# Performance work log

Measured on AMD Instinct MI355X. Metric: run time of the kernel, lower is better.

## Reference

```python
import jax, jax.numpy as jnp
import numpy as np

N = 131072
L = 300  # lan_vec_len

def _boxes(k):
    k1, k2, k3, k4 = jax.random.split(k, 4)
    x1 = jax.random.uniform(k1, (N,)) * 500.0
    y1 = jax.random.uniform(k2, (N,)) * 500.0
    w = 1.0 + jax.random.uniform(k3, (N,)) * 200.0
    h = 1.0 + jax.random.uniform(k4, (N,)) * 200.0
    return x1, y1, x1 + w, y1 + h

def setup_inputs() -> dict:
    key = jax.random.key(0)
    ks = jax.random.split(key, 10)
    sbj_vec = jax.random.normal(ks[0], (N, L), jnp.float32)
    obj_vec = jax.random.normal(ks[1], (N, L), jnp.float32)
    sx1, sy1, sx2, sy2 = _boxes(ks[2])
    ox1, oy1, ox2, oy2 = _boxes(ks[3])
    label = jax.random.randint(ks[4], (N,), 0, 2).astype(jnp.float32)
    misc = jax.random.uniform(ks[5], (N,))
    # rlts columns: [0:4 misc, 4 label, 5:9 sbj box, 9 misc, 10:14 obj box, 14 misc]
    rlts = jnp.stack([misc, misc, misc, misc, label,
                      sx1, sy1, sx2, sy2, misc,
                      ox1, oy1, ox2, oy2, misc], axis=1)
    spa_w = jax.random.normal(ks[6], (8, 1), jnp.float32) * 0.1
    spa_b = jnp.zeros((1,), jnp.float32)
    lan_w1 = jax.random.normal(ks[7], (2 * L, L), jnp.float32) * 0.05
    lan_b1 = jnp.zeros((L,), jnp.float32)
    lan_w2 = jax.random.normal(ks[8], (L, 1), jnp.float32) * 0.05
    lan_b2 = jnp.zeros((1,), jnp.float32)
    return {"sbj_vec": sbj_vec, "obj_vec": obj_vec, "rlts": rlts,
            "spa_w": spa_w, "spa_b": spa_b,
            "lan_w1": lan_w1, "lan_b1": lan_b1,
            "lan_w2": lan_w2, "lan_b2": lan_b2}

def _ext_box_feat(rlts):
    sb = rlts[:, 5:9]
    ob = rlts[:, 10:14]
    sw = sb[:, 2] - sb[:, 0]
    sh = sb[:, 3] - sb[:, 1]
    ow = ob[:, 2] - ob[:, 0]
    oh = ob[:, 3] - ob[:, 1]
    sbj = jnp.stack([(sb[:, 0] - ob[:, 0]) / sw,
                     (sb[:, 1] - ob[:, 1]) / sh,
                     jnp.log(sw / ow), jnp.log(sh / oh)], axis=1)
    obj = jnp.stack([(ob[:, 0] - sb[:, 0]) / ow,
                     (ob[:, 1] - sb[:, 1]) / oh,
                     jnp.log(ow / sw), jnp.log(oh / sh)], axis=1)
    return sbj, obj

def reference(sbj_vec, obj_vec, rlts, spa_w, spa_b, lan_w1, lan_b1, lan_w2, lan_b2):
    sbj_box, obj_box = _ext_box_feat(rlts)
    lan_feat = jnp.concatenate([sbj_vec, obj_vec], axis=1)        # [N, 2L]
    box_feat = jnp.concatenate([sbj_box, obj_box], axis=1)        # [N, 8]
    # lan_stream: ReLU -> (Dropout: identity in eval) -> Linear -> ReLU -> Linear
    h = jax.nn.relu(lan_feat)
    h = jax.nn.relu(h @ lan_w1 + lan_b1)
    lan_scores = h @ lan_w2 + lan_b2                              # [N, 1]
    box_scores = box_feat @ spa_w + spa_b                         # [N, 1]
    scores = jax.nn.sigmoid(lan_scores + box_scores)              # [N, 1]
    ys = (rlts[:, 4] > 0).astype(scores.dtype)                    # [N]
    s = scores[:, 0]
    # binary cross entropy (mean), clamped like torch's BCE
    log_s = jnp.clip(jnp.log(jnp.clip(s, 1e-12, 1.0)), -100.0)
    log_1s = jnp.clip(jnp.log(jnp.clip(1.0 - s, 1e-12, 1.0)), -100.0)
    loss = -jnp.mean(ys * log_s + (1.0 - ys) * log_1s)
    # faithful replication of loss_test's (buggy) counting logic, vectorized
    neg = ys == 0
    pos = ~neg
    N_pos = jnp.sum(pos.astype(jnp.float32))
    N_neg = jnp.sum(neg.astype(jnp.float32))
    N_pos_right = jnp.sum((neg & (s >= 0.5)).astype(jnp.float32))
    N_neg_right = jnp.sum((pos & (s < 0.5)).astype(jnp.float32))
    recall_pos = N_pos_right / N_pos
    recall_neg = N_neg_right / N_neg
    recall_all = (N_pos_right + N_neg_right) / (N_pos + N_neg)
    return scores, loss, recall_pos, recall_neg, recall_all
```

## Files before the change

### kernel.cpp

```cpp
#include <hip/hip_runtime.h>

constexpr int NROWS  = 131072;
constexpr int LDIM   = 300;
constexpr int KDIM   = 600;
constexpr int NPAD   = 320;
constexpr int KGRP   = 76;
constexpr int MTILE  = 64;
constexpr int NBLKS  = NROWS / MTILE;
constexpr int KSTEPS = 19;
constexpr int WT_ELEMS = KGRP * NPAD * 8;
constexpr size_t PART_OFF = 393216;
constexpr int ASTRIDE = 40;

typedef __bf16 bf16x8 __attribute__((ext_vector_type(8)));
typedef float  f32x4  __attribute__((ext_vector_type(4)));

__device__ __forceinline__ unsigned short f2bf(float f) {
    unsigned u = __float_as_uint(f);
    u += 0x7fffu + ((u >> 16) & 1u);
    return (unsigned short)(u >> 16);
}

__global__ void prep_w1(const float* __restrict__ w1, unsigned short* __restrict__ wt) {
    int idx = blockIdx.x * 256 + threadIdx.x;
    if (idx >= WT_ELEMS) return;
    int j    = idx & 7;
    int rest = idx >> 3;
    int n    = rest % NPAD;
    int kg   = rest / NPAD;
    int k    = kg * 8 + j;
    float v = 0.f;
    if (k < KDIM && n < LDIM) v = w1[k * LDIM + n];
    wt[idx] = f2bf(v);
}

__launch_bounds__(256, 3)
__global__ void main_kernel(const float* __restrict__ sbj, const float* __restrict__ obj,
                            const float* __restrict__ rlts,
                            const float* __restrict__ spa_w, const float* __restrict__ spa_b,
                            const float* __restrict__ b1, const float* __restrict__ w2,
                            const float* __restrict__ b2,
                            const unsigned short* __restrict__ wt,
                            float* __restrict__ out_scores, float* __restrict__ part) {
    __shared__ __attribute__((aligned(16))) short A_lds[2][MTILE * ASTRIDE];
    __shared__ float lanpart[4][MTILE];
    __shared__ float redbuf[4][8];

    const int tid  = threadIdx.x;
    const int lane = tid & 63;
    const int wv   = tid >> 6;
    const int l4   = lane & 15;
    const int q4   = lane >> 4;
    const int nbase = wv * 80;

    const int  blk  = blockIdx.x;
    const long row0 = (long)blk * MTILE;

    const int a_quad = tid & 7;
    const int a_row  = tid >> 3;

    f32x4 acc[4][5];
    #pragma unroll
    for (int rt = 0; rt < 4; ++rt)
        #pragma unroll
        for (int ct = 0; ct < 5; ++ct)
            acc[rt][ct] = (f32x4)(0.f);

    float4 pre[2];

    auto load_A = [&](int kt) {
        const int k0 = kt * 32 + a_quad * 4;
        #pragma unroll
        for (int i = 0; i < 2; ++i) {
            const long grow = row0 + a_row + i * 32;
            if (k0 < LDIM)       pre[i] = *(const float4*)(sbj + grow * LDIM + k0);
            else if (k0 < KDIM)  pre[i] = *(const float4*)(obj + grow * LDIM + (k0 - LDIM));
            else                 pre[i] = make_float4(0.f, 0.f, 0.f, 0.f);
        }
    };
    auto store_A = [&](int buf) {
        #pragma unroll
        for (int i = 0; i < 2; ++i) {
            const int row = a_row + i * 32;
            unsigned h0 = f2bf(fmaxf(pre[i].x, 0.f));
            unsigned h1 = f2bf(fmaxf(pre[i].y, 0.f));
            unsigned h2 = f2bf(fmaxf(pre[i].z, 0.f));
            unsigned h3 = f2bf(fmaxf(pre[i].w, 0.f));
            uint2 pk = make_uint2(h0 | (h1 << 16), h2 | (h3 << 16));
            *(uint2*)&A_lds[buf][row * ASTRIDE + a_quad * 4] = pk;
        }
    };

    load_A(0);
    store_A(0);

    for (int kt = 0; kt < KSTEPS; ++kt) {
        const int buf = kt & 1;
        __syncthreads();
        if (kt + 1 < KSTEPS) load_A(kt + 1);

        bf16x8 af[4];
        #pragma unroll
        for (int rt = 0; rt < 4; ++rt)
            af[rt] = *(const bf16x8*)&A_lds[buf][(rt * 16 + l4) * ASTRIDE + q4 * 8];

        bf16x8 bfr[5];
        #pragma unroll
        for (int ct = 0; ct < 5; ++ct) {
            const int kg = kt * 4 + q4;
            bfr[ct] = *(const bf16x8*)(wt + ((size_t)kg * NPAD + nbase + ct * 16 + l4) * 8);
        }
        #pragma unroll
        for (int ct = 0; ct < 5; ++ct)
            #pragma unroll
            for (int rt = 0; rt < 4; ++rt)
                acc[rt][ct] = __builtin_amdgcn_mfma_f32_16x16x32_bf16(af[rt], bfr[ct], acc[rt][ct], 0, 0, 0);

        if (kt + 1 < KSTEPS) store_A(buf ^ 1);
    }

    float part_r[4][4];
    #pragma unroll
    for (int rt = 0; rt < 4; ++rt)
        #pragma unroll
        for (int r = 0; r < 4; ++r) part_r[rt][r] = 0.f;

    #pragma unroll
    for (int ct = 0; ct < 5; ++ct) {
        const int n = nbase + ct * 16 + l4;
        if (n < LDIM) {
            const float b1n = b1[n];
            const float w2n = w2[n];
            #pragma unroll
            for (int rt = 0; rt < 4; ++rt)
                #pragma unroll
                for (int r = 0; r < 4; ++r) {
                    float h = fmaxf(acc[rt][ct][r] + b1n, 0.f);
                    part_r[rt][r] = fmaf(h, w2n, part_r[rt][r]);
                }
        }
    }
    #pragma unroll
    for (int off = 1; off < 16; off <<= 1)
        #pragma unroll
        for (int rt = 0; rt < 4; ++rt)
            #pragma unroll
            for (int r = 0; r < 4; ++r)
                part_r[rt][r] += __shfl_xor(part_r[rt][r], off, 64);

    if (l4 == 0) {
        #pragma unroll
        for (int rt = 0; rt < 4; ++rt)
            #pragma unroll
            for (int r = 0; r < 4; ++r)
                lanpart[wv][rt * 16 + q4 * 4 + r] = part_r[rt][r];
    }
    __syncthreads();

    float s_loss = 0.f, s_cp = 0.f, s_cn = 0.f, s_pr = 0.f, s_nr = 0.f;
    if (tid < MTILE) {
        const long g   = row0 + tid;
        const float lan = lanpart[0][tid] + lanpart[1][tid] + lanpart[2][tid] + lanpart[3][tid] + b2[0];
        const float* rr = rlts + g * 15;
        const float label = rr[4];
        const float sx1 = rr[5],  sy1 = rr[6],  sx2 = rr[7],  sy2 = rr[8];
        const float ox1 = rr[10], oy1 = rr[11], ox2 = rr[12], oy2 = rr[13];
        const float sw = sx2 - sx1, sh = sy2 - sy1, ow = ox2 - ox1, oh = oy2 - oy1;
        float bs = spa_w[0] * ((sx1 - ox1) / sw)
                 + spa_w[1] * ((sy1 - oy1) / sh)
                 + spa_w[2] * logf(sw / ow)
                 + spa_w[3] * logf(sh / oh)
                 + spa_w[4] * ((ox1 - sx1) / ow)
                 + spa_w[5] * ((oy1 - sy1) / oh)
                 + spa_w[6] * logf(ow / sw)
                 + spa_w[7] * logf(oh / sh)
                 + spa_b[0];
        const float z = lan + bs;
        const float s = 1.f / (1.f + expf(-z));
        out_scores[g] = s;
        const float ls = fmaxf(logf(fminf(fmaxf(s, 1e-12f), 1.f)), -100.f);
        const float l1 = fmaxf(logf(fminf(fmaxf(1.f - s, 1e-12f), 1.f)), -100.f);
        const bool ys = label > 0.f;
        s_loss = ys ? ls : l1;
        s_cp   = ys ? 1.f : 0.f;
        s_cn   = ys ? 0.f : 1.f;
        s_pr   = (!ys && s >= 0.5f) ? 1.f : 0.f;
        s_nr   = (ys && s < 0.5f)  ? 1.f : 0.f;
    }
    #pragma unroll
    for (int off = 1; off < 64; off <<= 1) {
        s_loss += __shfl_xor(s_loss, off, 64);
        s_cp   += __shfl_xor(s_cp, off, 64);
        s_cn   += __shfl_xor(s_cn, off, 64);
        s_pr   += __shfl_xor(s_pr, off, 64);
        s_nr   += __shfl_xor(s_nr, off, 64);
    }
    if (lane == 0) {
        redbuf[wv][0] = s_loss; redbuf[wv][1] = s_cp; redbuf[wv][2] = s_cn;
        redbuf[wv][3] = s_pr;   redbuf[wv][4] = s_nr;
    }
    __syncthreads();
    if (tid == 0) {
        float t0 = 0.f, t1 = 0.f, t2 = 0.f, t3 = 0.f, t4 = 0.f;
        for (int w = 0; w < 4; ++w) {
            t0 += redbuf[w][0]; t1 += redbuf[w][1]; t2 += redbuf[w][2];
            t3 += redbuf[w][3]; t4 += redbuf[w][4];
        }
        part[blk * 8 + 0] = t0; part[blk * 8 + 1] = t1; part[blk * 8 + 2] = t2;
        part[blk * 8 + 3] = t3; part[blk * 8 + 4] = t4;
    }
}

__global__ void final_reduce(const float* __restrict__ part, float* __restrict__ out) {
    __shared__ float red[4][8];
    const int tid = threadIdx.x;
    const int lane = tid & 63, wv = tid >> 6;
    float a0 = 0.f, a1 = 0.f, a2 = 0.f, a3 = 0.f, a4 = 0.f;
    for (int b = tid; b < NBLKS; b += 256) {
        a0 += part[b * 8 + 0]; a1 += part[b * 8 + 1]; a2 += part[b * 8 + 2];
        a3 += part[b * 8 + 3]; a4 += part[b * 8 + 4];
    }
    #pragma unroll
    for (int off = 1; off < 64; off <<= 1) {
        a0 += __shfl_xor(a0, off, 64); a1 += __shfl_xor(a1, off, 64);
        a2 += __shfl_xor(a2, off, 64); a3 += __shfl_xor(a3, off, 64);
        a4 += __shfl_xor(a4, off, 64);
    }
    if (lane == 0) { red[wv][0] = a0; red[wv][1] = a1; red[wv][2] = a2; red[wv][3] = a3; red[wv][4] = a4; }
    __syncthreads();
    if (tid == 0) {
        float t0 = 0.f, t1 = 0.f, t2 = 0.f, t3 = 0.f, t4 = 0.f;
        for (int w = 0; w < 4; ++w) {
            t0 += red[w][0]; t1 += red[w][1]; t2 += red[w][2]; t3 += red[w][3]; t4 += red[w][4];
        }
        out[NROWS + 0] = -t0 / (float)NROWS;
        out[NROWS + 1] = t3 / t1;
        out[NROWS + 2] = t4 / t2;
        out[NROWS + 3] = (t3 + t4) / (t1 + t2);
    }
}

extern "C" void kernel_launch(void* const* d_in, const int* in_sizes, int n_in,
                              void* d_out, int out_size, void* d_ws, size_t ws_size,
                              hipStream_t stream) {
    const float* sbj   = (const float*)d_in[0];
    const float* obj   = (const float*)d_in[1];
    const float* rlts  = (const float*)d_in[2];
    const float* spa_w = (const float*)d_in[3];
    const float* spa_b = (const float*)d_in[4];
    const float* w1    = (const float*)d_in[5];
    const float* b1    = (const float*)d_in[6];
    const float* w2    = (const float*)d_in[7];
    const float* b2    = (const float*)d_in[8];
    float* out = (float*)d_out;

    unsigned short* wt = (unsigned short*)d_ws;
    float* part = (float*)((char*)d_ws + PART_OFF);

    prep_w1<<<(WT_ELEMS + 255) / 256, 256, 0, stream>>>(w1, wt);
    main_kernel<<<NBLKS, 256, 0, stream>>>(sbj, obj, rlts, spa_w, spa_b, b1, w2, b2, wt, out, part);
    final_reduce<<<1, 256, 0, stream>>>(part, out);
}
```

Measured before the change: 385.0 us.

## Stage full A tile in LDS upfront and drop per-step barriers

Loads and converts the whole 64x600 activation tile into LDS (about 77 KB, k-grouped layout) in one pass before the MFMA loop, instead of double-buffering 32-wide K slices. This removes the per-K-step __syncthreads and register prefetch staging and puts all global loads in flight at once. The larger LDS footprint lowers occupancy, so launch bounds drop from 3 to 2 blocks per CU. The gain from fewer barriers may be offset because the load phase no longer overlaps with compute and fewer blocks are resident.

```diff
diff --git a/kernel.cpp b/kernel.cpp
--- a/kernel.cpp
+++ b/kernel.cpp
@@ -10,7 +10,6 @@
 constexpr int KSTEPS = 19;
 constexpr int WT_ELEMS = KGRP * NPAD * 8;
 constexpr size_t PART_OFF = 393216;
-constexpr int ASTRIDE = 40;
 
 typedef __bf16 bf16x8 __attribute__((ext_vector_type(8)));
 typedef float  f32x4  __attribute__((ext_vector_type(4)));
@@ -34,7 +33,7 @@
     wt[idx] = f2bf(v);
 }
 
-__launch_bounds__(256, 3)
+__launch_bounds__(256, 2)
 __global__ void main_kernel(const float* __restrict__ sbj, const float* __restrict__ obj,
                             const float* __restrict__ rlts,
                             const float* __restrict__ spa_w, const float* __restrict__ spa_b,
@@ -42,7 +41,7 @@
                             const float* __restrict__ b2,
                             const unsigned short* __restrict__ wt,
                             float* __restrict__ out_scores, float* __restrict__ part) {
-    __shared__ __attribute__((aligned(16))) short A_lds[2][MTILE * ASTRIDE];
+    __shared__ __attribute__((aligned(16))) unsigned short A_lds[KGRP * MTILE * 8];
     __shared__ float lanpart[4][MTILE];
     __shared__ float redbuf[4][8];
 
@@ -59,6 +58,27 @@
     const int a_quad = tid & 7;
     const int a_row  = tid >> 3;
 
+    #pragma unroll
+    for (int kc = 0; kc < KSTEPS; ++kc) {
+        const int k0 = kc * 32 + a_quad * 4;
+        const int kg = k0 >> 3;
+        const int j0 = k0 & 7;
+        #pragma unroll
+        for (int i = 0; i < 2; ++i) {
+            const int  row  = a_row + i * 32;
+            const long grow = row0 + row;
+            float4 v = make_float4(0.f, 0.f, 0.f, 0.f);
+            if (k0 < LDIM)       v = *(const float4*)(sbj + grow * LDIM + k0);
+            else if (k0 < KDIM)  v = *(const float4*)(obj + grow * LDIM + (k0 - LDIM));
+            unsigned h0 = f2bf(fmaxf(v.x, 0.f));
+            unsigned h1 = f2bf(fmaxf(v.y, 0.f));
+            unsigned h2 = f2bf(fmaxf(v.z, 0.f));
+            unsigned h3 = f2bf(fmaxf(v.w, 0.f));
+            uint2 pk = make_uint2(h0 | (h1 << 16), h2 | (h3 << 16));
+            *(uint2*)&A_lds[(kg * MTILE + row) * 8 + j0] = pk;
+        }
+    }
+
     f32x4 acc[4][5];
     #pragma unroll
     for (int rt = 0; rt < 4; ++rt)
@@ -66,57 +86,28 @@
         for (int ct = 0; ct < 5; ++ct)
             acc[rt][ct] = (f32x4)(0.f);
 
-    float4 pre[2];
-
-    auto load_A = [&](int kt) {
-        const int k0 = kt * 32 + a_quad * 4;
-        #pragma unroll
-        for (int i = 0; i < 2; ++i) {
-            const long grow = row0 + a_row + i * 32;
-            if (k0 < LDIM)       pre[i] = *(const float4*)(sbj + grow * LDIM + k0);
-            else if (k0 < KDIM)  pre[i] = *(const float4*)(obj + grow * LDIM + (k0 - LDIM));
-            else                 pre[i] = make_float4(0.f, 0.f, 0.f, 0.f);
-        }
-    };
-    auto store_A = [&](int buf) {
-        #pragma unroll
-        for (int i = 0; i < 2; ++i) {
-            const int row = a_row + i * 32;
-            unsigned h0 = f2bf(fmaxf(pre[i].x, 0.f));
-            unsigned h1 = f2bf(fmaxf(pre[i].y, 0.f));
-            unsigned h2 = f2bf(fmaxf(pre[i].z, 0.f));
-            unsigned h3 = f2bf(fmaxf(pre[i].w, 0.f));
-            uint2 pk = make_uint2(h0 | (h1 << 16), h2 | (h3 << 16));
-            *(uint2*)&A_lds[buf][row * ASTRIDE + a_quad * 4] = pk;
-        }
-    };
-
-    load_A(0);
-    store_A(0);
-
+    __syncthreads();
+
+    const int abase = q4 * 512 + l4 * 8;
+    const unsigned short* wbase = wt + ((size_t)q4 * NPAD + nbase + l4) * 8;
+
+    #pragma unroll
     for (int kt = 0; kt < KSTEPS; ++kt) {
-        const int buf = kt & 1;
-        __syncthreads();
-        if (kt + 1 < KSTEPS) load_A(kt + 1);
-
         bf16x8 af[4];
         #pragma unroll
         for (int rt = 0; rt < 4; ++rt)
-            af[rt] = *(const bf16x8*)&A_lds[buf][(rt * 16 + l4) * ASTRIDE + q4 * 8];
+            af[rt] = *(const bf16x8*)&A_lds[kt * 2048 + rt * 128 + abase];
 
         bf16x8 bfr[5];
         #pragma unroll
-        for (int ct = 0; ct < 5; ++ct) {
-            const int kg = kt * 4 + q4;
-            bfr[ct] = *(const bf16x8*)(wt + ((size_t)kg * NPAD + nbase + ct * 16 + l4) * 8);
-        }
+        for (int ct = 0; ct < 5; ++ct)
+            bfr[ct] = *(const bf16x8*)(wbase + (size_t)kt * 4 * NPAD * 8 + ct * 16 * 8);
+
         #pragma unroll
         for (int ct = 0; ct < 5; ++ct)
             #pragma unroll
             for (int rt = 0; rt < 4; ++rt)
                 acc[rt][ct] = __builtin_amdgcn_mfma_f32_16x16x32_bf16(af[rt], bfr[ct], acc[rt][ct], 0, 0, 0);
-
-        if (kt + 1 < KSTEPS) store_A(buf ^ 1);
     }
 
     float part_r[4][4];
```

Measured after the change: 401.4 us. 1.04x slower.
